# Kernel optimization log

Measured on AMD Instinct MI355X. Metric: run time of the kernel, lower is better.

The kernel has to match this reference:

```python
import jax, jax.numpy as jnp
import numpy as np

D = 1024
H = 16
HD = D // H  # 64

def setup_inputs() -> dict:
    key = jax.random.key(0)
    ks = jax.random.split(key, 7)
    B, S = 2, 2048
    x = jax.random.normal(ks[0], (B, S, D), dtype=jnp.float32)
    M = jax.random.randint(ks[1], (B, S, S), 0, 2, dtype=jnp.int32)
    s = 1.0 / np.sqrt(D)
    W_q = jax.random.normal(ks[2], (D, D), dtype=jnp.float32) * s
    W_k = jax.random.normal(ks[3], (D, D), dtype=jnp.float32) * s
    W_v = jax.random.normal(ks[4], (D, D), dtype=jnp.float32) * s
    W_o = jax.random.normal(ks[5], (D, D), dtype=jnp.float32) * s
    b_o = jax.random.normal(ks[6], (D,), dtype=jnp.float32) * 0.01
    return {"x": x, "M": M, "W_q": W_q, "W_k": W_k, "W_v": W_v, "W_o": W_o, "b_o": b_o}

def reference(x, M, W_q, W_k, W_v, W_o, b_o):
    B, S, _ = x.shape
    scale = HD ** -0.5
    # project and split heads: [B, H, S, HD]
    def heads(W):
        return (x @ W.T).reshape(B, S, H, HD).transpose(0, 2, 1, 3)
    Q, K, V = heads(W_q), heads(W_k), heads(W_v)
    scores = jnp.einsum('bhqd,bhkd->bhqk', Q, K) * scale
    mask = (M[:, None, :, :] == 0)  # broadcast over heads
    scores = jnp.where(mask, jnp.float32(-1e9), scores)
    A = jax.nn.softmax(scores, axis=-1)
    out = jnp.einsum('bhqk,bhkd->bhqd', A, V)
    out = out.transpose(0, 2, 1, 3).reshape(B, S, D)
    return out @ W_o.T + b_o
```

## Files before the change

### kernel.cpp

```cpp
#include <hip/hip_runtime.h>
#include <hip/hip_bf16.h>

typedef unsigned short u16;
typedef unsigned int u32;
typedef unsigned long long u64;
typedef _Float16 f16;
typedef __attribute__((__ext_vector_type__(4))) _Float16 f16x4;
typedef __attribute__((__ext_vector_type__(8))) short bf16x8;
typedef __attribute__((__ext_vector_type__(4))) float f32x4;
typedef __attribute__((__ext_vector_type__(16))) float f32x16;
typedef __attribute__((__ext_vector_type__(2))) int i32x2;

__device__ __forceinline__ u16 f2bf(float f) {
    u32 u = __float_as_uint(f);
    return (u16)((u + 0x7fffu + ((u >> 16) & 1u)) >> 16);
}

__global__ __launch_bounds__(256) void prep_kernel(
    const float4* __restrict__ x,  const float4* __restrict__ wq,
    const float4* __restrict__ wk, const float4* __restrict__ wv,
    const float4* __restrict__ wo,
    u16* __restrict__ xb, u16* __restrict__ wqb, u16* __restrict__ wkb,
    u16* __restrict__ wvb, u16* __restrict__ wob,
    const int* __restrict__ M, u64* __restrict__ Mb2)
{
    if (blockIdx.x < 8192) {
        int gid = blockIdx.x * 256 + threadIdx.x;
        const float4* src; u16* dst; int off;
        if (gid < 1048576) { src = x; dst = xb; off = gid; }
        else {
            int g = gid - 1048576;
            int sel = g >> 18;
            off = g & 262143;
            src = sel == 0 ? wq : sel == 1 ? wk : sel == 2 ? wv : wo;
            dst = sel == 0 ? wqb : sel == 1 ? wkb : sel == 2 ? wvb : wob;
        }
        float4 f = src[off];
        ushort4 o;
        o.x = f2bf(f.x); o.y = f2bf(f.y); o.z = f2bf(f.z); o.w = f2bf(f.w);
        ((ushort4*)dst)[off] = o;
    } else {
        int wg   = (blockIdx.x - 8192) * 4 + (threadIdx.x >> 6);
        int lane = threadIdx.x & 63;
        int w = wg & 31;
        int q = (wg >> 5) & 2047;
        int b = wg >> 16;
        size_t base = ((size_t)(b * 2048 + q)) * 2048 + w * 64 + lane;
        u64 bits = __ballot(M[base] != 0);
        if (lane == 0) Mb2[(size_t)(b * 32 + w) * 2048 + q] = bits;
    }
}

template<int MODE, int BN>
__global__ __launch_bounds__(256) void gemm_k(
    const u16* __restrict__ Ag, const u16* __restrict__ Bg,
    u16* __restrict__ Cq, u16* __restrict__ Kfr, u16* __restrict__ Vfr,
    float* __restrict__ Cf, const float* __restrict__ bias)
{
    constexpr int Kd = 1024;
    constexpr int NB = BN / 32;
    __shared__ u16 SM[8192 + BN * 64];
    u16* As0 = SM;
    u16* As1 = SM + 4096;
    u16* Bs0 = SM + 8192;
    u16* Bs1 = SM + 8192 + BN * 32;
    const int tid  = threadIdx.x;
    const int wave = tid >> 6, lane = tid & 63;
    const int quad = lane >> 4, l16 = lane & 15;
    const int n0 = blockIdx.x * BN;
    const int m0 = blockIdx.y * 128;

    const int wm = (wave & 1) * 64, wn = (wave >> 1) * (BN / 2);
    f32x4 acc[4][NB];
    #pragma unroll
    for (int i = 0; i < 4; i++)
        #pragma unroll
        for (int j = 0; j < NB; j++)
            acc[i][j] = (f32x4){0.f, 0.f, 0.f, 0.f};

    const int sr = lane >> 2;
    const int sk = (lane & 3) * 8;
    const int ca0 = wave * 2, ca1 = ca0 + 1;
    const u16* gA0 = Ag + (size_t)(m0 + ca0 * 16 + sr) * Kd + sk;
    const u16* gA1 = Ag + (size_t)(m0 + ca1 * 16 + sr) * Kd + sk;
    const int cb0 = (BN == 128) ? wave * 2 : wave;
    const u16* gB0 = Bg + (size_t)(n0 + cb0 * 16 + sr) * Kd + sk;
    const u16* gB1 = (BN == 128) ? Bg + (size_t)(n0 + (cb0 + 1) * 16 + sr) * Kd + sk : nullptr;

    #define GLL16(gp, lp) __builtin_amdgcn_global_load_lds( \
        (const __attribute__((address_space(1))) void*)(gp), \
        (__attribute__((address_space(3))) void*)(lp), 16, 0, 0)

    for (int k0 = 0; k0 < Kd; k0 += 64) {
        __syncthreads();
        GLL16(gA0 + k0, As0 + ca0 * 512);
        GLL16(gA1 + k0, As0 + ca1 * 512);
        GLL16(gB0 + k0, Bs0 + cb0 * 512);
        if (BN == 128) GLL16(gB1 + k0, Bs0 + (cb0 + 1) * 512);
        GLL16(gA0 + k0 + 32, As1 + ca0 * 512);
        GLL16(gA1 + k0 + 32, As1 + ca1 * 512);
        GLL16(gB0 + k0 + 32, Bs1 + cb0 * 512);
        if (BN == 128) GLL16(gB1 + k0 + 32, Bs1 + (cb0 + 1) * 512);
        __syncthreads();

        #pragma unroll
        for (int kk = 0; kk < 2; kk++) {
            const u16* Ah = kk ? As1 : As0;
            const u16* Bh = kk ? Bs1 : Bs0;
            bf16x8 af[4], bfr[NB];
            #pragma unroll
            for (int mb = 0; mb < 4; mb++)
                af[mb] = *(const bf16x8*)&Ah[(wm + mb * 16 + l16) * 32 + quad * 8];
            #pragma unroll
            for (int nb = 0; nb < NB; nb++)
                bfr[nb] = *(const bf16x8*)&Bh[(wn + nb * 16 + l16) * 32 + quad * 8];
            #pragma unroll
            for (int mb = 0; mb < 4; mb++)
                #pragma unroll
                for (int nb = 0; nb < NB; nb++)
                    acc[mb][nb] = __builtin_amdgcn_mfma_f32_16x16x32_bf16(
                        af[mb], bfr[nb], acc[mb][nb], 0, 0, 0);
        }
    }
    #undef GLL16

    if (MODE == 1) {
        #pragma unroll
        for (int mb = 0; mb < 4; mb++)
            #pragma unroll
            for (int nb = 0; nb < NB; nb++) {
                const int row = m0 + wm + mb * 16 + quad * 4;
                const int col = n0 + wn + nb * 16 + l16;
                #pragma unroll
                for (int r = 0; r < 4; r++)
                    Cf[(size_t)(row + r) * 1024 + col] = acc[mb][nb][r] + bias[col];
            }
        return;
    }

    const int region = n0 >> 10;
    if (region == 0) {
        #pragma unroll
        for (int mb = 0; mb < 4; mb++)
            #pragma unroll
            for (int nb = 0; nb < NB; nb++) {
                const int row = m0 + wm + mb * 16 + quad * 4;
                const int ccol = (n0 & 1023) + wn + nb * 16 + l16;
                #pragma unroll
                for (int r = 0; r < 4; r++)
                    Cq[(size_t)(row + r) * 1024 + ccol] =
                        f2bf(acc[mb][nb][r] * 0.18033688011112042f);
            }
        return;
    }

    const int bb = m0 >> 11;
    const int kt_base = (m0 & 2047) >> 6;
    const int head_base = (n0 & 1023) >> 6;
    u16* dst = (region == 1) ? Kfr : Vfr;
    #pragma unroll
    for (int pass = 0; pass < 2; pass++) {
        __syncthreads();
        #pragma unroll
        for (int mb = 0; mb < 4; mb++) {
            const int rowb = wm + mb * 16 + quad * 4;
            if ((rowb >> 6) != pass) continue;
            #pragma unroll
            for (int nb = 0; nb < NB; nb++) {
                const int ccol = wn + nb * 16 + l16;
                const int h2 = ccol >> 6, dd = ccol & 63;
                if (region == 1) {
                    const int t = dd >> 4, hik = (dd >> 3) & 1, j = dd & 7;
                    #pragma unroll
                    for (int r = 0; r < 4; r++) {
                        const int km = (rowb + r) & 63;
                        const int f = (km >> 5) * 4 + t;
                        const int lanek = hik * 32 + (km & 31);
                        SM[((h2 * 8 + f) * 64 + lanek) * 8 + j] = f2bf(acc[mb][nb][r]);
                    }
                } else {
                    const int kinb = rowb & 63;
                    const int t = kinb >> 4, hiv = (kinb >> 3) & 1, jb = kinb & 7;
                    const int f = (dd >> 5) * 4 + t;
                    const int lanev = hiv * 32 + (dd & 31);
                    ushort4 pk;
                    pk.x = f2bf(acc[mb][nb][0]); pk.y = f2bf(acc[mb][nb][1]);
                    pk.z = f2bf(acc[mb][nb][2]); pk.w = f2bf(acc[mb][nb][3]);
                    *(ushort4*)&SM[((h2 * 8 + f) * 64 + lanev) * 8 + jb] = pk;
                }
            }
        }
        __syncthreads();
        const int h2g = tid >> 7;
        const int inner = (tid & 127) * 32;
        const size_t gbase =
            ((size_t)(bb * 16 + head_base + h2g) * 32 + kt_base + pass) * 4096;
        #pragma unroll
        for (int c = 0; c < 4; c++)
            *(bf16x8*)&dst[gbase + inner + c * 8] =
                *(const bf16x8*)&SM[h2g * 4096 + inner + c * 8];
    }
}

__global__ __launch_bounds__(256, 2) void attn_kernel(
    const u16* __restrict__ Qg, const u16* __restrict__ Kfr, const u16* __restrict__ Vfr,
    const u64* __restrict__ Mb2, f16* __restrict__ Opart, float* __restrict__ Lpart)
{
    const int qt = blockIdx.x >> 1;
    const int kh = blockIdx.x & 1;
    const int h  = blockIdx.y;
    const int b  = blockIdx.z;
    const int tid = threadIdx.x, wave = tid >> 6, lane = tid & 63;
    const int l31 = lane & 31, hi = lane >> 5;

    const int qrow0 = qt * 256 + wave * 64;
    const int bh    = b * 16 + h;

    bf16x8 qfa[4], qfb[4];
    {
        const u16* qp = Qg + ((size_t)b * 2048 + qrow0 + l31) * 1024 + h * 64 + hi * 8;
        #pragma unroll
        for (int t = 0; t < 4; t++) qfa[t] = *(const bf16x8*)(qp + t * 16);
        #pragma unroll
        for (int t = 0; t < 4; t++) qfb[t] = *(const bf16x8*)(qp + 32 * 1024 + t * 16);
    }

    const u32 fro = (u32)bh * 131072u + (u32)lane * 8u;
    const u64* mp = Mb2 + (size_t)(b * 32) * 2048 + qrow0 + l31;

    bf16x8 ones;
    #pragma unroll
    for (int j = 0; j < 8; j++) ones[j] = (short)0x3F80;

    f32x16 oa0, oa1, ob0, ob1, la, lb;
    #pragma unroll
    for (int i = 0; i < 16; i++) {
        oa0[i] = 0.f; oa1[i] = 0.f; ob0[i] = 0.f; ob1[i] = 0.f;
        la[i] = 0.f;  lb[i] = 0.f;
    }

    const int kt0 = kh * 16;
    #pragma unroll 1
    for (int kt = kt0; kt < kt0 + 16; ++kt) {
        const u64 mwa = mp[(size_t)kt * 2048];
        const u64 mwb = mp[(size_t)kt * 2048 + 32];
        const u32 fb = fro + (u32)kt * 4096u;

        #pragma unroll
        for (int ph = 0; ph < 2; ph++) {
            bf16x8 kf[4], vf[4];
            #pragma unroll
            for (int t = 0; t < 4; t++)
                kf[t] = *(const bf16x8*)(Kfr + fb + (u32)(ph * 4 + t) * 512u);
            vf[0] = *(const bf16x8*)(Vfr + fb + (u32)(2 * ph) * 512u);
            vf[1] = *(const bf16x8*)(Vfr + fb + (u32)(2 * ph + 1) * 512u);
            vf[2] = *(const bf16x8*)(Vfr + fb + (u32)(4 + 2 * ph) * 512u);
            vf[3] = *(const bf16x8*)(Vfr + fb + (u32)(4 + 2 * ph + 1) * 512u);

            const u32 mna = ~((ph ? (u32)(mwa >> 32) : (u32)mwa) >> (hi * 4));
            const u32 mnb = ~((ph ? (u32)(mwb >> 32) : (u32)mwb) >> (hi * 4));
            f32x16 sa, sb;
            #pragma unroll
            for (int reg = 0; reg < 16; reg++) {
                const int kb2 = (reg & 3) + 8 * (reg >> 2);
                sa[reg] = __int_as_float(
                    __builtin_amdgcn_sbfe((int)mna, kb2, 1) & (int)0xFF800000);
                sb[reg] = __int_as_float(
                    __builtin_amdgcn_sbfe((int)mnb, kb2, 1) & (int)0xFF800000);
            }
            #pragma unroll
            for (int t = 0; t < 4; t++) {
                sa = __builtin_amdgcn_mfma_f32_32x32x16_bf16(kf[t], qfa[t], sa, 0, 0, 0);
                sb = __builtin_amdgcn_mfma_f32_32x32x16_bf16(kf[t], qfb[t], sb, 0, 0, 0);
            }

            u32 wa[8], wb[8];
            #pragma unroll
            for (int i = 0; i < 8; i++) {
                const float ea0 = __builtin_amdgcn_exp2f(sa[2 * i]);
                const float ea1 = __builtin_amdgcn_exp2f(sa[2 * i + 1]);
                wa[i] = __builtin_amdgcn_perm(__float_as_uint(ea1),
                                              __float_as_uint(ea0), 0x07060302u);
                const float eb0 = __builtin_amdgcn_exp2f(sb[2 * i]);
                const float eb1 = __builtin_amdgcn_exp2f(sb[2 * i + 1]);
                wb[i] = __builtin_amdgcn_perm(__float_as_uint(eb1),
                                              __float_as_uint(eb0), 0x07060302u);
            }

            bf16x8 pba[2], pbb[2];
            #pragma unroll
            for (int fl = 0; fl < 2; fl++) {
                i32x2 a02 = __builtin_amdgcn_permlane32_swap(
                    (int)wa[4 * fl + 0], (int)wa[4 * fl + 2], false, false);
                i32x2 a13 = __builtin_amdgcn_permlane32_swap(
                    (int)wa[4 * fl + 1], (int)wa[4 * fl + 3], false, false);
                union { u32 u[4]; bf16x8 v; } fa;
                fa.u[0] = (u32)a02[0]; fa.u[1] = (u32)a13[0];
                fa.u[2] = (u32)a02[1]; fa.u[3] = (u32)a13[1];
                pba[fl] = fa.v;
                i32x2 b02 = __builtin_amdgcn_permlane32_swap(
                    (int)wb[4 * fl + 0], (int)wb[4 * fl + 2], false, false);
                i32x2 b13 = __builtin_amdgcn_permlane32_swap(
                    (int)wb[4 * fl + 1], (int)wb[4 * fl + 3], false, false);
                union { u32 u[4]; bf16x8 v; } fbu;
                fbu.u[0] = (u32)b02[0]; fbu.u[1] = (u32)b13[0];
                fbu.u[2] = (u32)b02[1]; fbu.u[3] = (u32)b13[1];
                pbb[fl] = fbu.v;
            }

            oa0 = __builtin_amdgcn_mfma_f32_32x32x16_bf16(vf[0], pba[0], oa0, 0, 0, 0);
            ob0 = __builtin_amdgcn_mfma_f32_32x32x16_bf16(vf[0], pbb[0], ob0, 0, 0, 0);
            oa0 = __builtin_amdgcn_mfma_f32_32x32x16_bf16(vf[1], pba[1], oa0, 0, 0, 0);
            ob0 = __builtin_amdgcn_mfma_f32_32x32x16_bf16(vf[1], pbb[1], ob0, 0, 0, 0);
            oa1 = __builtin_amdgcn_mfma_f32_32x32x16_bf16(vf[2], pba[0], oa1, 0, 0, 0);
            ob1 = __builtin_amdgcn_mfma_f32_32x32x16_bf16(vf[2], pbb[0], ob1, 0, 0, 0);
            oa1 = __builtin_amdgcn_mfma_f32_32x32x16_bf16(vf[3], pba[1], oa1, 0, 0, 0);
            ob1 = __builtin_amdgcn_mfma_f32_32x32x16_bf16(vf[3], pbb[1], ob1, 0, 0, 0);
            la  = __builtin_amdgcn_mfma_f32_32x32x16_bf16(ones,  pba[0], la,  0, 0, 0);
            lb  = __builtin_amdgcn_mfma_f32_32x32x16_bf16(ones,  pbb[0], lb,  0, 0, 0);
            la  = __builtin_amdgcn_mfma_f32_32x32x16_bf16(ones,  pba[1], la,  0, 0, 0);
            lb  = __builtin_amdgcn_mfma_f32_32x32x16_bf16(ones,  pbb[1], lb,  0, 0, 0);
        }
    }

    const size_t obase = ((size_t)(kh * 32 + bh) * 2048 + qrow0 + l31) * 64;
    #pragma unroll
    for (int tile = 0; tile < 2; tile++) {
        #pragma unroll
        for (int g = 0; g < 4; g++) {
            const int d0 = tile * 32 + g * 8 + hi * 4;
            f16x4 pka, pkb;
            #pragma unroll
            for (int r = 0; r < 4; r++) {
                const int reg = g * 4 + r;
                pka[r] = (f16)(tile == 0 ? oa0[reg] : oa1[reg]);
                pkb[r] = (f16)(tile == 0 ? ob0[reg] : ob1[reg]);
            }
            *(f16x4*)&Opart[obase + d0] = pka;
            *(f16x4*)&Opart[obase + 32 * 64 + d0] = pkb;
        }
    }
    Lpart[(size_t)kh * 65536 + bh * 2048 + qrow0 + l31] = la[0];
    Lpart[(size_t)kh * 65536 + bh * 2048 + qrow0 + 32 + l31] = lb[0];
}

__global__ __launch_bounds__(256) void merge_kernel(
    const f16* __restrict__ Opart, const float* __restrict__ Lpart,
    u16* __restrict__ AO)
{
    const int gid = blockIdx.x * 256 + threadIdx.x;
    const int c4 = gid & 15;
    const int q  = (gid >> 4) & 2047;
    const int bh = gid >> 15;
    const int b  = bh >> 4, h = bh & 15;

    float l = 0.f;
    float s0 = 0.f, s1 = 0.f, s2 = 0.f, s3 = 0.f;
    #pragma unroll
    for (int k = 0; k < 2; k++) {
        const size_t pbase = ((size_t)(k * 32 + bh) * 2048 + q) * 64 + c4 * 4;
        f16x4 o = *(const f16x4*)&Opart[pbase];
        s0 += (float)o[0]; s1 += (float)o[1]; s2 += (float)o[2]; s3 += (float)o[3];
        l += Lpart[(size_t)k * 65536 + bh * 2048 + q];
    }
    const float inv = 1.0f / l;
    ushort4 o;
    o.x = f2bf(s0 * inv); o.y = f2bf(s1 * inv);
    o.z = f2bf(s2 * inv); o.w = f2bf(s3 * inv);
    *(ushort4*)&AO[((size_t)b * 2048 + q) * 1024 + h * 64 + c4 * 4] = o;
}

extern "C" void kernel_launch(void* const* d_in, const int* in_sizes, int n_in,
                              void* d_out, int out_size, void* d_ws, size_t ws_size,
                              hipStream_t stream)
{
    const float* x  = (const float*)d_in[0];
    const int*   Mm = (const int*)d_in[1];
    const float* Wq = (const float*)d_in[2];
    const float* Wk = (const float*)d_in[3];
    const float* Wv = (const float*)d_in[4];
    const float* Wo = (const float*)d_in[5];
    const float* bo = (const float*)d_in[6];
    float* out = (float*)d_out;

    u16* ws  = (u16*)d_ws;
    u16* xb  = ws;
    u16* wqb = xb  + 4194304;
    u16* wkb = wqb + 1048576;
    u16* wvb = wkb + 1048576;
    u16* wob = wvb + 1048576;
    u16* Qb  = wob + 1048576;
    u16* Kfr = Qb  + 4194304;
    u16* Vfr = Kfr + 4194304;
    u16* AOb = Vfr + 4194304;
    u64* Mb2 = (u64*)(AOb + 4194304);
    f16* Opart = (f16*)(Mb2 + 131072);
    float* Lpart = (float*)(Opart + 8388608);

    prep_kernel<<<40960, 256, 0, stream>>>(
        (const float4*)x, (const float4*)Wq, (const float4*)Wk,
        (const float4*)Wv, (const float4*)Wo, xb, wqb, wkb, wvb, wob,
        Mm, Mb2);

    dim3 g1(24, 32, 1);
    gemm_k<0, 128><<<g1, 256, 0, stream>>>(xb, wqb, Qb, Kfr, Vfr, nullptr, nullptr);

    dim3 g2(16, 16, 2);
    attn_kernel<<<g2, 256, 0, stream>>>(Qb, Kfr, Vfr, Mb2, Opart, Lpart);

    merge_kernel<<<4096, 256, 0, stream>>>(Opart, Lpart, AOb);

    dim3 g3(16, 32, 1);
    gemm_k<1, 64><<<g3, 256, 0, stream>>>(AOb, wob, nullptr, nullptr, nullptr,
                                          out, bo);
}
```

Before: 235.5 us.

## Fuse split-K attention merge into attention kernel via intra-block LDS reduction

The attention kernel no longer splits the key range across separate blocks. Each block now handles 128 query rows, and within a block, pairs of waves split the key range between them. Partial outputs and row sums are combined in shared memory, then normalized and written directly as bf16. This removes the separate merge kernel launch and the f16/f32 partial-result round trip through global memory. The cost is extra LDS, a block-wide barrier, and half the waves idling during the final normalize-and-store.

```diff
diff --git a/kernel.cpp b/kernel.cpp
--- a/kernel.cpp
+++ b/kernel.cpp
@@ -204,16 +204,17 @@
 
 __global__ __launch_bounds__(256, 2) void attn_kernel(
     const u16* __restrict__ Qg, const u16* __restrict__ Kfr, const u16* __restrict__ Vfr,
-    const u64* __restrict__ Mb2, f16* __restrict__ Opart, float* __restrict__ Lpart)
+    const u64* __restrict__ Mb2, u16* __restrict__ AO)
 {
-    const int qt = blockIdx.x >> 1;
-    const int kh = blockIdx.x & 1;
+    const int qt = blockIdx.x;
     const int h  = blockIdx.y;
     const int b  = blockIdx.z;
     const int tid = threadIdx.x, wave = tid >> 6, lane = tid & 63;
     const int l31 = lane & 31, hi = lane >> 5;
-
-    const int qrow0 = qt * 256 + wave * 64;
+    const int pair = wave >> 1;
+    const int kh   = wave & 1;
+
+    const int qrow0 = qt * 128 + pair * 64;
     const int bh    = b * 16 + h;
 
     bf16x8 qfa[4], qfb[4];
@@ -323,51 +324,50 @@
         }
     }
 
-    const size_t obase = ((size_t)(kh * 32 + bh) * 2048 + qrow0 + l31) * 64;
-    #pragma unroll
-    for (int tile = 0; tile < 2; tile++) {
-        #pragma unroll
-        for (int g = 0; g < 4; g++) {
-            const int d0 = tile * 32 + g * 8 + hi * 4;
-            f16x4 pka, pkb;
-            #pragma unroll
-            for (int r = 0; r < 4; r++) {
-                const int reg = g * 4 + r;
-                pka[r] = (f16)(tile == 0 ? oa0[reg] : oa1[reg]);
-                pkb[r] = (f16)(tile == 0 ? ob0[reg] : ob1[reg]);
-            }
-            *(f16x4*)&Opart[obase + d0] = pka;
-            *(f16x4*)&Opart[obase + 32 * 64 + d0] = pkb;
-        }
-    }
-    Lpart[(size_t)kh * 65536 + bh * 2048 + qrow0 + l31] = la[0];
-    Lpart[(size_t)kh * 65536 + bh * 2048 + qrow0 + 32 + l31] = lb[0];
-}
-
-__global__ __launch_bounds__(256) void merge_kernel(
-    const f16* __restrict__ Opart, const float* __restrict__ Lpart,
-    u16* __restrict__ AO)
-{
-    const int gid = blockIdx.x * 256 + threadIdx.x;
-    const int c4 = gid & 15;
-    const int q  = (gid >> 4) & 2047;
-    const int bh = gid >> 15;
-    const int b  = bh >> 4, h = bh & 15;
-
-    float l = 0.f;
-    float s0 = 0.f, s1 = 0.f, s2 = 0.f, s3 = 0.f;
-    #pragma unroll
-    for (int k = 0; k < 2; k++) {
-        const size_t pbase = ((size_t)(k * 32 + bh) * 2048 + q) * 64 + c4 * 4;
-        f16x4 o = *(const f16x4*)&Opart[pbase];
-        s0 += (float)o[0]; s1 += (float)o[1]; s2 += (float)o[2]; s3 += (float)o[3];
-        l += Lpart[(size_t)k * 65536 + bh * 2048 + q];
-    }
-    const float inv = 1.0f / l;
-    ushort4 o;
-    o.x = f2bf(s0 * inv); o.y = f2bf(s1 * inv);
-    o.z = f2bf(s2 * inv); o.w = f2bf(s3 * inv);
-    *(ushort4*)&AO[((size_t)b * 2048 + q) * 1024 + h * 64 + c4 * 4] = o;
+    __shared__ float MRG[2 * 64 * 68];
+    float* slot = &MRG[(pair * 64 + lane) * 68];
+    if (kh == 1) {
+        #pragma unroll
+        for (int i = 0; i < 4; i++) {
+            *(f32x4*)(slot +      4 * i) = (f32x4){oa0[4*i], oa0[4*i+1], oa0[4*i+2], oa0[4*i+3]};
+            *(f32x4*)(slot + 16 + 4 * i) = (f32x4){oa1[4*i], oa1[4*i+1], oa1[4*i+2], oa1[4*i+3]};
+            *(f32x4*)(slot + 32 + 4 * i) = (f32x4){ob0[4*i], ob0[4*i+1], ob0[4*i+2], ob0[4*i+3]};
+            *(f32x4*)(slot + 48 + 4 * i) = (f32x4){ob1[4*i], ob1[4*i+1], ob1[4*i+2], ob1[4*i+3]};
+        }
+        slot[64] = la[0];
+        slot[65] = lb[0];
+    }
+    __syncthreads();
+    if (kh == 0) {
+        #pragma unroll
+        for (int i = 0; i < 16; i++) {
+            oa0[i] += slot[i];
+            oa1[i] += slot[16 + i];
+            ob0[i] += slot[32 + i];
+            ob1[i] += slot[48 + i];
+        }
+        const float invA = 1.0f / (la[0] + slot[64]);
+        const float invB = 1.0f / (lb[0] + slot[65]);
+        const size_t qbase = ((size_t)b * 2048 + qrow0 + l31) * 1024 + h * 64;
+        #pragma unroll
+        for (int tile = 0; tile < 2; tile++) {
+            #pragma unroll
+            for (int g = 0; g < 4; g++) {
+                const int d0 = tile * 32 + g * 8 + hi * 4;
+                ushort4 pa, pb;
+                #pragma unroll
+                for (int r = 0; r < 4; r++) {
+                    const int reg = g * 4 + r;
+                    const float va = (tile == 0 ? oa0[reg] : oa1[reg]) * invA;
+                    const float vb = (tile == 0 ? ob0[reg] : ob1[reg]) * invB;
+                    ((u16*)&pa)[r] = f2bf(va);
+                    ((u16*)&pb)[r] = f2bf(vb);
+                }
+                *(ushort4*)&AO[qbase + d0] = pa;
+                *(ushort4*)&AO[qbase + (size_t)32 * 1024 + d0] = pb;
+            }
+        }
+    }
 }
 
 extern "C" void kernel_launch(void* const* d_in, const int* in_sizes, int n_in,
@@ -394,8 +394,6 @@
     u16* Vfr = Kfr + 4194304;
     u16* AOb = Vfr + 4194304;
     u64* Mb2 = (u64*)(AOb + 4194304);
-    f16* Opart = (f16*)(Mb2 + 131072);
-    float* Lpart = (float*)(Opart + 8388608);
 
     prep_kernel<<<40960, 256, 0, stream>>>(
         (const float4*)x, (const float4*)Wq, (const float4*)Wk,
@@ -406,9 +404,7 @@
     gemm_k<0, 128><<<g1, 256, 0, stream>>>(xb, wqb, Qb, Kfr, Vfr, nullptr, nullptr);
 
     dim3 g2(16, 16, 2);
-    attn_kernel<<<g2, 256, 0, stream>>>(Qb, Kfr, Vfr, Mb2, Opart, Lpart);
-
-    merge_kernel<<<4096, 256, 0, stream>>>(Opart, Lpart, AOb);
+    attn_kernel<<<g2, 256, 0, stream>>>(Qb, Kfr, Vfr, Mb2, AOb);
 
     dim3 g3(16, 32, 1);
     gemm_k<1, 64><<<g3, 256, 0, stream>>>(AOb, wob, nullptr, nullptr, nullptr,
```

Result: no change. 232.6 us (-1.2%).
